# Performance work log

Measured on AMD Instinct MI355X. Metric: run time of the kernel, lower is better.

## Reference

```python
import jax, jax.numpy as jnp
import numpy as np

N, D_IN, D_OUT, E = 4096, 4096, 4096, 8

def setup_inputs() -> dict:
    key = jax.random.key(0)
    k1, k2, k3 = jax.random.split(key, 3)
    scale_in = 1.0 / np.sqrt(D_IN)
    x = jax.random.normal(k1, (N, D_IN), dtype=jnp.float32)
    gate_w = jax.random.normal(k2, (D_IN, E), dtype=jnp.float32) * scale_in
    gate_b = jnp.zeros((E,), dtype=jnp.float32)
    expert_w = jax.random.normal(k3, (E, D_IN, D_OUT), dtype=jnp.float32) * scale_in
    expert_b = jnp.zeros((E, D_OUT), dtype=jnp.float32)
    return {"x": x, "gate_w": gate_w, "gate_b": gate_b,
            "expert_w": expert_w, "expert_b": expert_b}

def reference(x, gate_w, gate_b, expert_w, expert_b):
    # gate scores: [N, E]
    gate = jax.nn.softmax(x @ gate_w + gate_b, axis=-1)
    # all experts run on every token: [E, N, D_OUT]
    expert_out = jnp.einsum('nd,edr->enr', x, expert_w) + expert_b[:, None, :]
    # gate-weighted combine: [N, D_OUT]
    out = jnp.einsum('ne,enr->nr', gate, expert_out)
    return out
```

## Files before the change

### kernel.cpp

```cpp
#include <hip/hip_runtime.h>
#include <hip/hip_bf16.h>


typedef __attribute__((ext_vector_type(8))) short short8;
typedef __attribute__((ext_vector_type(4))) float f32x4;

#define NROWS 4096
#define DIN   4096
#define DOUT  4096
#define NEXP  8
#define KTOT  (NEXP * DIN)

__device__ __forceinline__ unsigned short f2b(float f) {
  unsigned int u = __float_as_uint(f);
  u += 0x7FFFu + ((u >> 16) & 1u);
  return (unsigned short)(u >> 16);
}

__device__ __forceinline__ void gload_lds16(const unsigned short* g, unsigned short* l) {
  __builtin_amdgcn_global_load_lds(
      (const __attribute__((address_space(1))) unsigned int*)(unsigned long long)g,
      (__attribute__((address_space(3))) unsigned int*)(unsigned int)(unsigned long long)l,
      16, 0, 0);
}

__global__ __launch_bounds__(256) void gate_kernel(const float* __restrict__ x,
                                                   const float* __restrict__ gw,
                                                   const float* __restrict__ gb,
                                                   float* __restrict__ g,
                                                   unsigned short* __restrict__ xb) {
  __shared__ float red[256][8];
  const int n = blockIdx.x, t = threadIdx.x;
  float a[8] = {0, 0, 0, 0, 0, 0, 0, 0};
  for (int d = t; d < DIN; d += 256) {
    float xv = x[(size_t)n * DIN + d];
    xb[(size_t)n * DIN + d] = f2b(xv);
    const float4* gwp = (const float4*)(gw + (size_t)d * 8);
    float4 w0 = gwp[0], w1 = gwp[1];
    a[0] += xv * w0.x; a[1] += xv * w0.y; a[2] += xv * w0.z; a[3] += xv * w0.w;
    a[4] += xv * w1.x; a[5] += xv * w1.y; a[6] += xv * w1.z; a[7] += xv * w1.w;
  }
  for (int e = 0; e < 8; ++e) red[t][e] = a[e];
  __syncthreads();
  for (int s = 128; s > 0; s >>= 1) {
    if (t < s)
      for (int e = 0; e < 8; ++e) red[t][e] += red[t + s][e];
    __syncthreads();
  }
  if (t == 0) {
    float l[8], m = -1e30f, ssum = 0.f;
    for (int e = 0; e < 8; ++e) { l[e] = red[0][e] + gb[e]; m = fmaxf(m, l[e]); }
    for (int e = 0; e < 8; ++e) { l[e] = expf(l[e] - m); ssum += l[e]; }
    for (int e = 0; e < 8; ++e) g[(size_t)n * 8 + e] = l[e] / ssum;
  }
}

__global__ __launch_bounds__(256) void transpose_w(const float* __restrict__ W,
                                                   unsigned short* __restrict__ bt) {
  __shared__ unsigned short tile[64][72];
  const int t = threadIdx.x;
  const int k0 = blockIdx.x * 64, r0 = blockIdx.y * 64;
  #pragma unroll
  for (int i = 0; i < 4; ++i) {
    int lin = i * 256 + t;
    int kr = lin >> 4, rq = (lin & 15) * 4;
    float4 v = *(const float4*)(W + (size_t)(k0 + kr) * 4096 + r0 + rq);
    tile[rq + 0][kr] = f2b(v.x);
    tile[rq + 1][kr] = f2b(v.y);
    tile[rq + 2][kr] = f2b(v.z);
    tile[rq + 3][kr] = f2b(v.w);
  }
  __syncthreads();
  #pragma unroll
  for (int i = 0; i < 2; ++i) {
    int lin = i * 256 + t;
    int rr = lin >> 3, kc = (lin & 7) * 8;
    uint4 v = *(const uint4*)&tile[rr][kc];
    *(uint4*)(bt + (size_t)(r0 + rr) * KTOT + k0 + kc) = v;
  }
}

__global__ __launch_bounds__(256) void gemm_moe(const unsigned short* __restrict__ xb,
                                                const unsigned short* __restrict__ bt,
                                                const float* __restrict__ gate,
                                                const float* __restrict__ eb,
                                                float* __restrict__ out) {
  __shared__ alignas(16) unsigned short sA[128 * 64];
  __shared__ alignas(16) unsigned short sB[128 * 64];
  __shared__ float sG[128 * 8];
  __shared__ float sBias[8 * 128];

  const int t = threadIdx.x;
  const int lane = t & 63;
  const int w = t >> 6;
  const int wm = w >> 1, wn = w & 1;

  const int bid = blockIdx.x;
  const int grp = bid >> 6, wi = bid & 63;
  const int row0 = ((grp >> 2) * 8 + (wi >> 3)) * 128;
  const int col0 = ((grp & 3) * 8 + (wi & 7)) * 128;

  #pragma unroll
  for (int i = 0; i < 4; ++i) {
    int lin = i * 256 + t;
    sG[lin] = gate[(size_t)row0 * 8 + lin];
    sBias[lin] = eb[(size_t)(lin >> 7) * DOUT + col0 + (lin & 127)];
  }

  const int laneRow = lane >> 3;
  const int swzK8 = (((lane & 7) ^ laneRow) * 8);
  const int mrow = lane & 15;
  const int quad = lane >> 4;

  f32x4 acc[4][4];
  #pragma unroll
  for (int i = 0; i < 4; ++i)
    #pragma unroll
    for (int j = 0; j < 4; ++j) acc[i][j] = (f32x4){0.f, 0.f, 0.f, 0.f};

  const size_t aRowBase = (size_t)(row0 + w * 32 + laneRow) * DIN;
  const size_t bRowBase = (size_t)(col0 + w * 32 + laneRow) * KTOT;

  for (int kt = 0; kt < KTOT / 64; ++kt) {
    const int k0 = kt * 64;
    const int kx = k0 & (DIN - 1);
    #pragma unroll
    for (int j = 0; j < 4; ++j) {
      gload_lds16(xb + aRowBase + (size_t)j * 8 * DIN + kx + swzK8,
                  &sA[(w * 32 + j * 8) * 64]);
      gload_lds16(bt + bRowBase + (size_t)j * 8 * KTOT + k0 + swzK8,
                  &sB[(w * 32 + j * 8) * 64]);
    }
    __syncthreads();

    #pragma unroll
    for (int kk = 0; kk < 2; ++kk) {
      short8 af[4], bf[4];
      #pragma unroll
      for (int i = 0; i < 4; ++i) {
        const int R = wm * 64 + i * 16 + mrow;
        af[i] = *(const short8*)&sA[R * 64 + (((kk << 2) + quad) ^ (mrow & 7)) * 8];
      }
      #pragma unroll
      for (int j = 0; j < 4; ++j) {
        const int R = wn * 64 + j * 16 + mrow;
        bf[j] = *(const short8*)&sB[R * 64 + (((kk << 2) + quad) ^ (mrow & 7)) * 8];
      }
      #pragma unroll
      for (int i = 0; i < 4; ++i)
        #pragma unroll
        for (int j = 0; j < 4; ++j)
          acc[i][j] = __builtin_amdgcn_mfma_f32_16x16x32_bf16(af[i], bf[j], acc[i][j], 0, 0, 0);
    }
    __syncthreads();

    if ((kt & 63) == 63 && kt != (KTOT / 64 - 1)) {
      const int e = kt >> 6;
      #pragma unroll
      for (int i = 0; i < 4; ++i) {
        #pragma unroll
        for (int r = 0; r < 4; ++r) {
          const int row_l = wm * 64 + i * 16 + quad * 4 + r;
          const float s = sG[row_l * 8 + e] / sG[row_l * 8 + e + 1];
          #pragma unroll
          for (int j = 0; j < 4; ++j) acc[i][j][r] *= s;
        }
      }
    }
  }

  #pragma unroll
  for (int i = 0; i < 4; ++i) {
    #pragma unroll
    for (int r = 0; r < 4; ++r) {
      const int row_l = wm * 64 + i * 16 + quad * 4 + r;
      float gv[8];
      #pragma unroll
      for (int e = 0; e < 8; ++e) gv[e] = sG[row_l * 8 + e];
      #pragma unroll
      for (int j = 0; j < 4; ++j) {
        const int col_l = wn * 64 + j * 16 + mrow;
        float bias = 0.f;
        #pragma unroll
        for (int e = 0; e < 8; ++e) bias += gv[e] * sBias[e * 128 + col_l];
        out[(size_t)(row0 + row_l) * DOUT + col0 + col_l] = acc[i][j][r] * gv[7] + bias;
      }
    }
  }
}

__global__ __launch_bounds__(256) void moe_fallback(const float* __restrict__ x,
                                                    const float* __restrict__ gw,
                                                    const float* __restrict__ gb,
                                                    const float* __restrict__ W,
                                                    const float* __restrict__ eb,
                                                    float* __restrict__ out) {
  __shared__ float sX[64][33];
  __shared__ float sW[32][65];
  __shared__ float sLog[64][8];
  __shared__ float sGate[64][8];
  const int t = threadIdx.x;
  const int r0 = blockIdx.y * 64, c0 = blockIdx.x * 64;

  const int grow = t & 63, epair = t >> 6;
  float lg0 = gb[2 * epair], lg1 = gb[2 * epair + 1];
  for (int d0 = 0; d0 < DIN; d0 += 32) {
    for (int i = 0; i < 8; ++i) {
      int lin = i * 256 + t, rr = lin >> 5, cc = lin & 31;
      sX[rr][cc] = x[(size_t)(r0 + rr) * DIN + d0 + cc];
    }
    __syncthreads();
    for (int dd = 0; dd < 32; ++dd) {
      float xv = sX[grow][dd];
      lg0 += xv * gw[(size_t)(d0 + dd) * 8 + 2 * epair];
      lg1 += xv * gw[(size_t)(d0 + dd) * 8 + 2 * epair + 1];
    }
    __syncthreads();
  }
  sLog[grow][2 * epair] = lg0;
  sLog[grow][2 * epair + 1] = lg1;
  __syncthreads();
  if (t < 64) {
    float m = -1e30f, s = 0.f, ex[8];
    for (int e = 0; e < 8; ++e) m = fmaxf(m, sLog[t][e]);
    for (int e = 0; e < 8; ++e) { ex[e] = expf(sLog[t][e] - m); s += ex[e]; }
    for (int e = 0; e < 8; ++e) sGate[t][e] = ex[e] / s;
  }
  __syncthreads();

  const int tr = t >> 4, tc = t & 15;
  float acc[4][4] = {};
  for (int e = 0; e < NEXP; ++e) {
    float part[4][4] = {};
    for (int d0 = 0; d0 < DIN; d0 += 32) {
      for (int i = 0; i < 8; ++i) {
        int lin = i * 256 + t, rr = lin >> 5, cc = lin & 31;
        sX[rr][cc] = x[(size_t)(r0 + rr) * DIN + d0 + cc];
      }
      for (int i = 0; i < 8; ++i) {
        int lin = i * 256 + t, dd = lin >> 6, cc = lin & 63;
        sW[dd][cc] = W[(size_t)e * DIN * DOUT + (size_t)(d0 + dd) * DOUT + c0 + cc];
      }
      __syncthreads();
      for (int dd = 0; dd < 32; ++dd) {
        float xa[4], wb[4];
        for (int i = 0; i < 4; ++i) xa[i] = sX[tr + 16 * i][dd];
        for (int j = 0; j < 4; ++j) wb[j] = sW[dd][tc + 16 * j];
        for (int i = 0; i < 4; ++i)
          for (int j = 0; j < 4; ++j) part[i][j] += xa[i] * wb[j];
      }
      __syncthreads();
    }
    for (int i = 0; i < 4; ++i) {
      float g = sGate[tr + 16 * i][e];
      for (int j = 0; j < 4; ++j)
        acc[i][j] += g * (part[i][j] + eb[(size_t)e * DOUT + c0 + tc + 16 * j]);
    }
  }
  for (int i = 0; i < 4; ++i)
    for (int j = 0; j < 4; ++j)
      out[(size_t)(r0 + tr + 16 * i) * DOUT + c0 + tc + 16 * j] = acc[i][j];
}

extern "C" void kernel_launch(void* const* d_in, const int* in_sizes, int n_in,
                              void* d_out, int out_size, void* d_ws, size_t ws_size,
                              hipStream_t stream) {
  const float* x  = (const float*)d_in[0];
  const float* gw = (const float*)d_in[1];
  const float* gb = (const float*)d_in[2];
  const float* W  = (const float*)d_in[3];
  const float* eb = (const float*)d_in[4];
  float* out = (float*)d_out;

  const size_t sz_xb = (size_t)NROWS * DIN * 2;
  const size_t sz_bt = (size_t)DOUT * KTOT * 2;
  const size_t sz_g  = (size_t)NROWS * 8 * 4;
  const size_t need = sz_xb + sz_bt + sz_g;

  if (ws_size >= need) {
    unsigned short* xb = (unsigned short*)d_ws;
    unsigned short* bt = (unsigned short*)((char*)d_ws + sz_xb);
    float* gate = (float*)((char*)d_ws + sz_xb + sz_bt);
    gate_kernel<<<NROWS, 256, 0, stream>>>(x, gw, gb, gate, xb);
    transpose_w<<<dim3(KTOT / 64, DOUT / 64), 256, 0, stream>>>(W, bt);
    gemm_moe<<<(NROWS / 128) * (DOUT / 128), 256, 0, stream>>>(xb, bt, gate, eb, out);
  } else {
    moe_fallback<<<dim3(DOUT / 64, NROWS / 64), 256, 0, stream>>>(x, gw, gb, W, eb, out);
  }
}
```

Baseline: 2.148 ms.

## Use 256x256 tiles with 4-slot LDS ring and prefetch-ahead pipelined GEMM

Rewrites the fused MoE GEMM to use 256x256 output tiles with 512 threads (8 waves, each 128x64), BK=32 and a 4-slot LDS ring. Global-to-LDS loads run two tiles ahead, so one barrier per tile replaces the two syncthreads. It also adds s_setprio around the MFMA block and remaps blocks across XCDs. The aim is more operand reuse per byte loaded and overlap of memory latency with MFMA work, at the cost of higher register and LDS pressure and only 256 workgroups.

```diff
diff --git a/kernel.cpp b/kernel.cpp
--- a/kernel.cpp
+++ b/kernel.cpp
@@ -80,100 +80,122 @@
   }
 }
 
-__global__ __launch_bounds__(256) void gemm_moe(const unsigned short* __restrict__ xb,
-                                                const unsigned short* __restrict__ bt,
-                                                const float* __restrict__ gate,
-                                                const float* __restrict__ eb,
-                                                float* __restrict__ out) {
-  __shared__ alignas(16) unsigned short sA[128 * 64];
-  __shared__ alignas(16) unsigned short sB[128 * 64];
-  __shared__ float sG[128 * 8];
-  __shared__ float sBias[8 * 128];
+#define BM 256
+#define BN 256
+#define BKK 32
+#define NTILES (KTOT / BKK)
+#define SLOT_SH 8192
+
+__global__ __launch_bounds__(512, 2) void gemm_moe(const unsigned short* __restrict__ xb,
+                                                   const unsigned short* __restrict__ bt,
+                                                   const float* __restrict__ gate,
+                                                   const float* __restrict__ eb,
+                                                   float* __restrict__ out) {
+  __shared__ alignas(16) unsigned short sA[4 * SLOT_SH];
+  __shared__ alignas(16) unsigned short sB[4 * SLOT_SH];
+  __shared__ float sG[256 * 8];
+  __shared__ float sBias[8 * 256];
 
   const int t = threadIdx.x;
   const int lane = t & 63;
   const int w = t >> 6;
-  const int wm = w >> 1, wn = w & 1;
+  const int wm = w >> 2;
+  const int wn = w & 3;
 
   const int bid = blockIdx.x;
-  const int grp = bid >> 6, wi = bid & 63;
-  const int row0 = ((grp >> 2) * 8 + (wi >> 3)) * 128;
-  const int col0 = ((grp & 3) * 8 + (wi & 7)) * 128;
+  const int wg = (bid & 7) * 32 + (bid >> 3);
+  const int tn = wg >> 4;
+  const int tm = wg & 15;
+  const int row0 = tm * BM;
+  const int col0 = tn * BN;
 
   #pragma unroll
   for (int i = 0; i < 4; ++i) {
-    int lin = i * 256 + t;
+    int lin = i * 512 + t;
     sG[lin] = gate[(size_t)row0 * 8 + lin];
-    sBias[lin] = eb[(size_t)(lin >> 7) * DOUT + col0 + (lin & 127)];
-  }
-
-  const int laneRow = lane >> 3;
-  const int swzK8 = (((lane & 7) ^ laneRow) * 8);
+    sBias[lin] = eb[(size_t)(lin >> 8) * DOUT + col0 + (lin & 255)];
+  }
+
   const int mrow = lane & 15;
   const int quad = lane >> 4;
-
-  f32x4 acc[4][4];
-  #pragma unroll
-  for (int i = 0; i < 4; ++i)
+  const int rs = (quad ^ ((mrow >> 1) & 3)) * 8;
+
+  f32x4 acc[8][4];
+  #pragma unroll
+  for (int i = 0; i < 8; ++i)
     #pragma unroll
     for (int j = 0; j < 4; ++j) acc[i][j] = (f32x4){0.f, 0.f, 0.f, 0.f};
 
-  const size_t aRowBase = (size_t)(row0 + w * 32 + laneRow) * DIN;
-  const size_t bRowBase = (size_t)(col0 + w * 32 + laneRow) * KTOT;
-
-  for (int kt = 0; kt < KTOT / 64; ++kt) {
-    const int k0 = kt * 64;
-    const int kx = k0 & (DIN - 1);
+  auto stage = [&](int T, int s) {
+    const int kA = (T * BKK) & (DIN - 1);
+    const int kB = T * BKK;
+    #pragma unroll
+    for (int r = 0; r < 2; ++r) {
+      const int row = r * 128 + w * 16 + (lane >> 2);
+      const int srcg = (lane & 3) ^ ((row >> 1) & 3);
+      gload_lds16(xb + (size_t)(row0 + row) * DIN + kA + srcg * 8,
+                  &sA[s * SLOT_SH + (r * 512 + w * 64) * 8]);
+      gload_lds16(bt + (size_t)(col0 + row) * KTOT + kB + srcg * 8,
+                  &sB[s * SLOT_SH + (r * 512 + w * 64) * 8]);
+    }
+  };
+
+  stage(0, 0);
+  stage(1, 1);
+  asm volatile("s_waitcnt vmcnt(4)" ::: "memory");
+  __builtin_amdgcn_s_barrier();
+
+  for (int T = 0; T < NTILES; ++T) {
+    const int s = T & 3;
+
+    if (T < NTILES - 2) stage(T + 2, (T + 2) & 3);
+
+    short8 af[8], bf[4];
+    #pragma unroll
+    for (int i = 0; i < 8; ++i) {
+      const int row = wm * 128 + i * 16 + mrow;
+      af[i] = *(const short8*)&sA[s * SLOT_SH + row * 32 + rs];
+    }
     #pragma unroll
     for (int j = 0; j < 4; ++j) {
-      gload_lds16(xb + aRowBase + (size_t)j * 8 * DIN + kx + swzK8,
-                  &sA[(w * 32 + j * 8) * 64]);
-      gload_lds16(bt + bRowBase + (size_t)j * 8 * KTOT + k0 + swzK8,
-                  &sB[(w * 32 + j * 8) * 64]);
-    }
-    __syncthreads();
-
-    #pragma unroll
-    for (int kk = 0; kk < 2; ++kk) {
-      short8 af[4], bf[4];
+      const int row = wn * 64 + j * 16 + mrow;
+      bf[j] = *(const short8*)&sB[s * SLOT_SH + row * 32 + rs];
+    }
+
+    __builtin_amdgcn_s_setprio(1);
+    #pragma unroll
+    for (int i = 0; i < 8; ++i)
       #pragma unroll
-      for (int i = 0; i < 4; ++i) {
-        const int R = wm * 64 + i * 16 + mrow;
-        af[i] = *(const short8*)&sA[R * 64 + (((kk << 2) + quad) ^ (mrow & 7)) * 8];
-      }
-      #pragma unroll
-      for (int j = 0; j < 4; ++j) {
-        const int R = wn * 64 + j * 16 + mrow;
-        bf[j] = *(const short8*)&sB[R * 64 + (((kk << 2) + quad) ^ (mrow & 7)) * 8];
-      }
-      #pragma unroll
-      for (int i = 0; i < 4; ++i)
+      for (int j = 0; j < 4; ++j)
+        acc[i][j] = __builtin_amdgcn_mfma_f32_16x16x32_bf16(af[i], bf[j], acc[i][j], 0, 0, 0);
+    __builtin_amdgcn_s_setprio(0);
+
+    if (T < NTILES - 1) {
+      if (T < NTILES - 2) asm volatile("s_waitcnt vmcnt(4)" ::: "memory");
+      else                asm volatile("s_waitcnt vmcnt(0)" ::: "memory");
+      __builtin_amdgcn_s_barrier();
+
+      if ((T & 127) == 127) {
+        const int e = T >> 7;
         #pragma unroll
-        for (int j = 0; j < 4; ++j)
-          acc[i][j] = __builtin_amdgcn_mfma_f32_16x16x32_bf16(af[i], bf[j], acc[i][j], 0, 0, 0);
-    }
-    __syncthreads();
-
-    if ((kt & 63) == 63 && kt != (KTOT / 64 - 1)) {
-      const int e = kt >> 6;
-      #pragma unroll
-      for (int i = 0; i < 4; ++i) {
-        #pragma unroll
-        for (int r = 0; r < 4; ++r) {
-          const int row_l = wm * 64 + i * 16 + quad * 4 + r;
-          const float s = sG[row_l * 8 + e] / sG[row_l * 8 + e + 1];
+        for (int i = 0; i < 8; ++i) {
           #pragma unroll
-          for (int j = 0; j < 4; ++j) acc[i][j][r] *= s;
+          for (int r = 0; r < 4; ++r) {
+            const int row_l = wm * 128 + i * 16 + quad * 4 + r;
+            const float sc = sG[row_l * 8 + e] / sG[row_l * 8 + e + 1];
+            #pragma unroll
+            for (int j = 0; j < 4; ++j) acc[i][j][r] *= sc;
+          }
         }
       }
     }
   }
 
   #pragma unroll
-  for (int i = 0; i < 4; ++i) {
+  for (int i = 0; i < 8; ++i) {
     #pragma unroll
     for (int r = 0; r < 4; ++r) {
-      const int row_l = wm * 64 + i * 16 + quad * 4 + r;
+      const int row_l = wm * 128 + i * 16 + quad * 4 + r;
       float gv[8];
       #pragma unroll
       for (int e = 0; e < 8; ++e) gv[e] = sG[row_l * 8 + e];
@@ -182,7 +204,7 @@
         const int col_l = wn * 64 + j * 16 + mrow;
         float bias = 0.f;
         #pragma unroll
-        for (int e = 0; e < 8; ++e) bias += gv[e] * sBias[e * 128 + col_l];
+        for (int e = 0; e < 8; ++e) bias += gv[e] * sBias[e * 256 + col_l];
         out[(size_t)(row0 + row_l) * DOUT + col0 + col_l] = acc[i][j][r] * gv[7] + bias;
       }
     }
@@ -283,7 +305,7 @@
     float* gate = (float*)((char*)d_ws + sz_xb + sz_bt);
     gate_kernel<<<NROWS, 256, 0, stream>>>(x, gw, gb, gate, xb);
     transpose_w<<<dim3(KTOT / 64, DOUT / 64), 256, 0, stream>>>(W, bt);
-    gemm_moe<<<(NROWS / 128) * (DOUT / 128), 256, 0, stream>>>(xb, bt, gate, eb, out);
+    gemm_moe<<<(NROWS / BM) * (DOUT / BN), 512, 0, stream>>>(xb, bt, gate, eb, out);
   } else {
     moe_fallback<<<dim3(DOUT / 64, NROWS / 64), 256, 0, stream>>>(x, gw, gb, W, eb, out);
   }
```

Result: faster. 1.748 ms (-18.6%).
